# Kernel optimization log

Measured on AMD Instinct MI355X. Metric: run time of the kernel, lower is better.

## Reference

```python
import jax, jax.numpy as jnp
import numpy as np

N = 50000      # nodes
E = 800000     # edges (avg degree 16)
D_IN = 369     # input feature dim
D = 128        # output_dim / GGNN hidden
T = 13         # max_edge_types
STEPS = 8      # GRU propagation steps
G = 256        # graphs in batch


def setup_inputs() -> dict:
    key = jax.random.key(0)
    ks = jax.random.split(key, 13)
    s = 0.05
    return {
        "x": jax.random.normal(ks[0], (N, D_IN), jnp.float32),
        "edge_index": jax.random.randint(ks[1], (2, E), 0, N, dtype=jnp.int64),
        "edge_attr": jax.random.randint(ks[2], (E,), 0, T, dtype=jnp.int64),
        "batch": jnp.sort(jax.random.randint(ks[3], (N,), 0, G, dtype=jnp.int64)),
        "lin_w": jax.random.normal(ks[4], (D_IN, D), jnp.float32) * s,
        "lin_b": jax.random.normal(ks[5], (D,), jnp.float32) * s,
        # per-edge-type GatedGraphConv: weight[t, step] is [D, D]
        "ggnn_w": jax.random.normal(ks[6], (T, STEPS, D, D), jnp.float32) * s,
        # per-edge-type GRUCell params (torch layout: [3*D, D] rows = r,z,n)
        "gru_w_ih": jax.random.normal(ks[7], (T, 3 * D, D), jnp.float32) * s,
        "gru_w_hh": jax.random.normal(ks[8], (T, 3 * D, D), jnp.float32) * s,
        "gru_b_ih": jax.random.normal(ks[9], (T, 3 * D), jnp.float32) * s,
        "gru_b_hh": jax.random.normal(ks[10], (T, 3 * D), jnp.float32) * s,
        "cls_w": jax.random.normal(ks[11], (D, 2), jnp.float32) * s,
        "cls_b": jax.random.normal(ks[12], (2,), jnp.float32) * s,
    }


def reference(x, edge_index, edge_attr, batch,
              lin_w, lin_b, ggnn_w, gru_w_ih, gru_w_hh, gru_b_ih, gru_b_hh,
              cls_w, cls_b):
    n_nodes = x.shape[0]
    h0 = x @ lin_w + lin_b                     # [N, D]; dropout omitted (eval)
    src, dst = edge_index[0], edge_index[1]

    messages = jnp.zeros_like(h0)
    for t in range(T):                          # fixed small set of edge types
        emask = (edge_attr == t).astype(h0.dtype)   # [E] select edges of this type
        w_ih, w_hh = gru_w_ih[t], gru_w_hh[t]
        b_ih, b_hh = gru_b_ih[t], gru_b_hh[t]

        def step(h, w):
            # message passing: aggregate (h @ w)[src] at dst over type-t edges
            xw = h @ w                           # [N, D]
            m = jax.ops.segment_sum(xw[src] * emask[:, None], dst,
                                    num_segments=n_nodes)
            # GRUCell(m, h)
            gi = m @ w_ih.T + b_ih               # [N, 3D]
            gh = h @ w_hh.T + b_hh
            ir, iz, i_n = jnp.split(gi, 3, axis=-1)
            hr, hz, h_n = jnp.split(gh, 3, axis=-1)
            r = jax.nn.sigmoid(ir + hr)
            z = jax.nn.sigmoid(iz + hz)
            n = jnp.tanh(i_n + r * h_n)
            return (1.0 - z) * n + z * h, None

        h_t, _ = jax.lax.scan(step, h0, ggnn_w[t])   # 8 steps
        messages = messages + h_t

    # global_mean_pool over graphs
    sums = jax.ops.segment_sum(messages, batch, num_segments=G)   # [G, D]
    counts = jax.ops.segment_sum(jnp.ones((n_nodes,), messages.dtype), batch,
                                 num_segments=G)
    pooled = sums / jnp.maximum(counts, 1.0)[:, None]
    return pooled @ cls_w + cls_b                                 # [G, 2]
```

## Files before the change

kernel.cpp:

```cpp
#include <hip/hip_runtime.h>
#include <hip/hip_bf16.h>
#include <stdint.h>

typedef __attribute__((ext_vector_type(8))) short   short8;
typedef __attribute__((ext_vector_type(8))) __bf16  bf16x8;
typedef __attribute__((ext_vector_type(4))) float   f32x4;

#define DEV __device__ __forceinline__

DEV float bf2f(uint16_t u){ union{uint32_t i; float f;} v; v.i = ((uint32_t)u)<<16; return v.f; }
DEV uint16_t f2bf(float f){ union{float f; uint32_t i;} v; v.f=f; uint32_t x=v.i;
  return (uint16_t)((x + 0x7fffu + ((x>>16)&1u))>>16); }
DEV float sigmf(float x){ return 1.0f/(1.0f + __expf(-x)); }
DEV float tanhx(float x){ x = fminf(15.f, fmaxf(-15.f, x)); float e = __expf(-2.0f*x);
  return (1.0f-e)/(1.0f+e); }

DEV bf16x8 as_bf(short8 s){ union{ short8 s; bf16x8 b; } u; u.s = s; return u.b; }
DEV f32x4 mfma16(short8 a, short8 b, f32x4 c){
  return __builtin_amdgcn_mfma_f32_16x16x32_bf16(as_bf(a), as_bf(b), c, 0, 0, 0);
}
DEV f32x4 vzero(){ f32x4 v; v[0]=0.f; v[1]=0.f; v[2]=0.f; v[3]=0.f; return v; }

__global__ void cast_bf16_kernel(const float* __restrict__ in, uint16_t* __restrict__ out, int n){
  int i = blockIdx.x*256 + threadIdx.x;
  if (i < n) out[i] = f2bf(in[i]);
}

__global__ void cast_swz_kernel(const float* __restrict__ in, uint16_t* __restrict__ out, int n){
  int i = blockIdx.x*256 + threadIdx.x;
  if (i < n){
    int k = i & 127, row = i >> 7;
    out[(row<<7) + (((k>>3) ^ (row&15))<<3) + (k&7)] = f2bf(in[i]);
  }
}

__global__ void xpad_kernel(const float* __restrict__ x, uint16_t* __restrict__ xb, int rows){
  int i = blockIdx.x*256 + threadIdx.x;
  if (i < rows*384){
    int r = i/384, c = i - r*384;
    xb[i] = (c < 369) ? f2bf(x[r*369 + c]) : (uint16_t)0;
  }
}

__global__ void lwt_kernel(const float* __restrict__ lw, uint16_t* __restrict__ lwT){
  int i = blockIdx.x*256 + threadIdx.x;
  if (i < 128*384){
    int nn = i/384, k = i - nn*384;
    lwT[i] = (k < 369) ? f2bf(lw[k*128 + nn]) : (uint16_t)0;
  }
}

__global__ __launch_bounds__(256,2)
void gemm_bt_kernel(const uint16_t* __restrict__ A, const uint16_t* __restrict__ B,
                    uint16_t* __restrict__ C,
                    int lda, int ldb, int M, int K4,
                    const float* __restrict__ bias, int swz,
                    long sA, long sB, long sC, int divA)
{
  int by = blockIdx.y;
  A += (long)(by/divA)*sA; B += (long)by*sB; C += (long)by*sC;
  int tid = threadIdx.x, lane = tid&63, wave = tid>>6;
  int l15 = lane&15, quad = lane>>4;
  int m0 = blockIdx.x*64 + wave*16;
  f32x4 acc[8];
  #pragma unroll
  for (int nf=0; nf<8; ++nf) acc[nf] = vzero();
  int mrow = min(m0 + l15, M-1);
  const char* arow = (const char*)(A + (long)mrow*lda) + quad*16;
  for (int kk=0; kk<K4; ++kk){
    short8 a = *(const short8*)(arow + kk*64);
    #pragma unroll
    for (int nf=0; nf<8; ++nf){
      const char* brow = (const char*)(B + (long)(nf*16+l15)*ldb) + quad*16;
      short8 b = *(const short8*)(brow + kk*64);
      acc[nf] = mfma16(a, b, acc[nf]);
    }
  }
  #pragma unroll
  for (int nf=0; nf<8; ++nf){
    int col = nf*16 + l15;
    float bb = bias ? bias[col] : 0.0f;
    #pragma unroll
    for (int i=0; i<4; ++i){
      int row = m0 + quad*4 + i;
      if (row < M){
        float v = acc[nf][i] + bb;
        int idx = swz ? (row*128 + (((col>>3)^(row&15))<<3) + (col&7)) : (row*128+col);
        C[idx] = f2bf(v);
      }
    }
  }
}

__global__ void edge_count_kernel(const int* __restrict__ ei, const int* __restrict__ ea,
                                  int* __restrict__ cnt, int E, int n){
  int e = blockIdx.x*256 + threadIdx.x;
  if (e < E){
    int dst = ei[E + e];
    int t = ea[e];
    atomicAdd(&cnt[t*n + dst], 1);
  }
}

__global__ void csr_alloc_kernel(const int* __restrict__ cnt, int* __restrict__ row_start,
                                 int* __restrict__ cursor, int* __restrict__ total, int R){
  __shared__ int wsum[4];
  __shared__ int base;
  int i = blockIdx.x*256 + threadIdx.x;
  int c = (i < R) ? cnt[i] : 0;
  int lane = threadIdx.x & 63, wave = threadIdx.x >> 6;
  int x = c;
  #pragma unroll
  for (int d=1; d<64; d<<=1){ int y = __shfl_up(x, d, 64); if (lane >= d) x += y; }
  if (lane == 63) wsum[wave] = x;
  __syncthreads();
  if (threadIdx.x == 0){
    int s0=wsum[0], s1=wsum[1], s2=wsum[2], s3=wsum[3];
    base = atomicAdd(total, s0+s1+s2+s3);
    wsum[0]=0; wsum[1]=s0; wsum[2]=s0+s1; wsum[3]=s0+s1+s2;
  }
  __syncthreads();
  int st = base + wsum[wave] + (x - c);
  if (i < R){ row_start[i] = st; cursor[i] = st; }
}

__global__ void edge_fill_kernel(const int* __restrict__ ei, const int* __restrict__ ea,
                                 int* __restrict__ cursor, int* __restrict__ csr, int E, int n){
  int e = blockIdx.x*256 + threadIdx.x;
  if (e < E){
    int src = ei[e], dst = ei[E+e], t = ea[e];
    int pos = atomicAdd(&cursor[t*n + dst], 1);
    csr[pos] = src;
  }
}

__global__ __launch_bounds__(256, 2)
void ggnn_step_kernel(const uint16_t* __restrict__ h_in_b,
                      uint16_t* __restrict__ h_out_b,
                      const uint16_t* __restrict__ W1_b,
                      const uint16_t* __restrict__ W2_b,
                      const float* __restrict__ bih_b,
                      const float* __restrict__ bhh_b,
                      const int* __restrict__ row_start_b,
                      const int* __restrict__ row_cnt_b,
                      const int* __restrict__ csr_src,
                      int n, int s, int t_off,
                      long hin_stride, long hout_stride)
{
  __shared__ __align__(16) uint16_t sB[128*128];
  const int t = t_off + blockIdx.y;
  const uint16_t* h_in  = h_in_b  + (long)blockIdx.y*hin_stride;
  uint16_t*       h_out = h_out_b + (long)blockIdx.y*hout_stride;
  const uint16_t* W1s = W1_b + (size_t)(t*8+s)*384*128;
  const uint16_t* W2s = W2_b + (size_t)t*384*128;
  const float* bih = bih_b + t*384;
  const float* bhh = bhh_b + t*384;

  const int tid = threadIdx.x, lane = tid&63, wave = tid>>6;
  const int l15 = lane&15, quad = lane>>4;
  const int rbase = blockIdx.x*64;
  const int ar = rbase + wave*16 + l15;
  const int arc = min(ar, n-1);

  const uint16_t* stp[6] = { W1s, W2s, W1s+2*16384, W2s+2*16384, W1s+16384, W2s+16384 };

  short8 tmp[8];
  {
    const char* g = (const char*)stp[0] + tid*16;
    #pragma unroll
    for (int it=0; it<8; ++it) tmp[it] = *(const short8*)(g + it*4096);
  }

  short8 hfr[4];
  {
    const short8* hrow = (const short8*)(h_in + (long)arc*128);
    #pragma unroll
    for (int kk=0; kk<4; ++kk) hfr[kk] = hrow[kk*4 + quad];
  }

  float acc[32];
  #pragma unroll
  for (int j=0; j<32; ++j) acc[j] = 0.f;
  if (ar < n){
    int st = row_start_b[(size_t)t*n + ar];
    int cn = row_cnt_b  [(size_t)t*n + ar];
    for (int e=0; e<cn; ++e){
      int src = csr_src[st+e];
      const short8* sr = (const short8*)(h_in + (long)src*128);
      #pragma unroll
      for (int kk=0; kk<4; ++kk){
        short8 hv = sr[kk*4+quad];
        #pragma unroll
        for (int j=0; j<8; ++j) acc[kk*8+j] += bf2f((uint16_t)hv[j]);
      }
    }
  }
  short8 afr[4];
  #pragma unroll
  for (int kk=0; kk<4; ++kk){
    #pragma unroll
    for (int j=0; j<8; ++j) afr[kk][j] = (short)f2bf(acc[kk*8+j]);
  }

  auto mma = [&](f32x4* a8, const short8* frag){
    #pragma unroll
    for (int kk=0; kk<4; ++kk){
      int ch = ((kk*4+quad)^l15)<<4;
      short8 a = frag[kk];
      #pragma unroll
      for (int nf=0; nf<8; ++nf){
        short8 b = *(const short8*)((const char*)sB + (nf*16+l15)*256 + ch);
        a8[nf] = mfma16(a, b, a8[nf]);
      }
    }
  };

  f32x4 rg[8], nng[8], zg[8];
  #pragma unroll
  for (int nf=0; nf<8; ++nf){ rg[nf]=vzero(); nng[nf]=vzero(); zg[nf]=vzero(); }

  #pragma unroll
  for (int g=0; g<6; ++g){
    __syncthreads();
    {
      char* l = (char*)sB + tid*16;
      #pragma unroll
      for (int it=0; it<8; ++it) *(short8*)(l + it*4096) = tmp[it];
    }
    __syncthreads();
    if (g < 5){
      const char* gp = (const char*)stp[g+1] + tid*16;
      #pragma unroll
      for (int it=0; it<8; ++it) tmp[it] = *(const short8*)(gp + it*4096);
    }
    if (g == 0)      mma(rg, afr);
    else if (g == 1){
      mma(rg, hfr);
      #pragma unroll
      for (int nf=0; nf<8; ++nf){
        int col = nf*16 + l15;
        float bs = bih[col] + bhh[col];
        #pragma unroll
        for (int i=0; i<4; ++i) rg[nf][i] = sigmf(rg[nf][i] + bs);
      }
    }
    else if (g == 2) mma(nng, afr);
    else if (g == 3){
      f32x4 nh[8];
      #pragma unroll
      for (int nf=0; nf<8; ++nf) nh[nf] = vzero();
      mma(nh, hfr);
      #pragma unroll
      for (int nf=0; nf<8; ++nf){
        int col = nf*16 + l15;
        float bin = bih[256+col], bhn = bhh[256+col];
        #pragma unroll
        for (int i=0; i<4; ++i)
          nng[nf][i] = tanhx(nng[nf][i] + bin + rg[nf][i]*(nh[nf][i] + bhn));
      }
    }
    else if (g == 4) mma(zg, afr);
    else             mma(zg, hfr);
  }

  #pragma unroll
  for (int nf=0; nf<8; ++nf){
    int col = nf*16 + l15;
    float bs = bih[128+col] + bhh[128+col];
    #pragma unroll
    for (int i=0; i<4; ++i){
      int row = rbase + wave*16 + quad*4 + i;
      if (row < n){
        float z = sigmf(zg[nf][i] + bs);
        float hv = bf2f(h_in[(long)row*128 + col]);
        float hnew = nng[nf][i] + z*(hv - nng[nf][i]);
        h_out[(long)row*128 + col] = f2bf(hnew);
      }
    }
  }
}

__global__ void reduce_kernel(const uint16_t* __restrict__ hfin, float* __restrict__ messages,
                              long stride, int nt, int accumulate, int total8){
  int i = blockIdx.x*256 + threadIdx.x;
  if (i < total8){
    float acc[8];
    #pragma unroll
    for (int j=0;j<8;++j) acc[j] = 0.f;
    if (accumulate){
      #pragma unroll
      for (int j=0;j<8;++j) acc[j] = messages[(long)i*8 + j];
    }
    for (int t=0; t<nt; ++t){
      short8 v = *(const short8*)(hfin + (long)t*stride + (long)i*8);
      #pragma unroll
      for (int j=0;j<8;++j) acc[j] += bf2f((uint16_t)v[j]);
    }
    #pragma unroll
    for (int j=0;j<8;++j) messages[(long)i*8 + j] = acc[j];
  }
}

__global__ void pool_kernel(const float* __restrict__ messages, const int* __restrict__ batch,
                            float* __restrict__ sums, int* __restrict__ cntg, int n){
  int id = blockIdx.x*256 + threadIdx.x;
  int col = id & 127;
  int nb = (id >> 7) * 8;
  float acc = 0.f; int curg = -1; int ccount = 0;
  for (int j=0; j<8; ++j){
    int node = nb + j;
    if (node < n){
      int g = batch[node];
      if (g != curg){
        if (curg >= 0){
          atomicAdd(&sums[curg*128+col], acc);
          if (col == 0) atomicAdd(&cntg[curg], ccount);
        }
        curg = g; acc = 0.f; ccount = 0;
      }
      acc += messages[(long)node*128 + col];
      ccount++;
    }
  }
  if (curg >= 0){
    atomicAdd(&sums[curg*128+col], acc);
    if (col == 0) atomicAdd(&cntg[curg], ccount);
  }
}

__global__ void classify_kernel(const float* __restrict__ sums, const int* __restrict__ cntg,
                                const float* __restrict__ cls_w, const float* __restrict__ cls_b,
                                float* __restrict__ out, int G){
  int g = threadIdx.x;
  if (g < G){
    float inv = 1.0f / fmaxf((float)cntg[g], 1.0f);
    float o0 = 0.f, o1 = 0.f;
    for (int d=0; d<128; ++d){
      float p = sums[g*128+d]*inv;
      o0 += p*cls_w[d*2];
      o1 += p*cls_w[d*2+1];
    }
    out[g*2]   = o0 + cls_b[0];
    out[g*2+1] = o1 + cls_b[1];
  }
}

extern "C" void kernel_launch(void* const* d_in, const int* in_sizes, int n_in,
                              void* d_out, int out_size, void* d_ws, size_t ws_size,
                              hipStream_t stream)
{
  const float* x      = (const float*)d_in[0];
  const int*   ei     = (const int*)d_in[1];
  const int*   ea     = (const int*)d_in[2];
  const int*   batch  = (const int*)d_in[3];
  const float* lin_w  = (const float*)d_in[4];
  const float* lin_b  = (const float*)d_in[5];
  const float* ggnn_w = (const float*)d_in[6];
  const float* w_ih   = (const float*)d_in[7];
  const float* w_hh   = (const float*)d_in[8];
  const float* b_ih   = (const float*)d_in[9];
  const float* b_hh   = (const float*)d_in[10];
  const float* cls_w  = (const float*)d_in[11];
  const float* cls_b  = (const float*)d_in[12];
  float* out = (float*)d_out;

  const int N = in_sizes[3];
  const int E = in_sizes[2];
  const int T = in_sizes[9] / 384;
  const int G = out_size / 2;
  const int STEPS = 8;

  struct Layout {
    float *messages, *sums; int *cntg, *total;
    int *cnt, *row_start, *csr;
    uint16_t *W2t, *W1t, *h0;
    uint16_t *hTA, *hTB;
    int *cursor; uint16_t *xb, *lwT, *gwb, *wihb;
    size_t zero_off, zero_len, end;
  };
  auto make_layout = [&](int nh)->Layout{
    Layout L; char* base = (char*)d_ws; char* p = base;
    auto A = [&](size_t b)->char*{ char* r = p; p += (b + 255) & ~(size_t)255; return r; };
    L.messages  = (float*)A((size_t)N*128*4);
    char* z0 = p;
    L.sums      = (float*)A((size_t)G*128*4);
    L.cntg      = (int*)  A((size_t)G*4);
    L.total     = (int*)  A(256);
    L.zero_off = (size_t)(z0 - base); L.zero_len = (size_t)(p - z0);
    L.cnt       = (int*)  A((size_t)T*N*4);
    L.row_start = (int*)  A((size_t)T*N*4);
    L.csr       = (int*)  A((size_t)E*4);
    L.W2t       = (uint16_t*)A((size_t)T*384*128*2);
    L.W1t       = (uint16_t*)A((size_t)T*8*384*128*2);
    L.h0        = (uint16_t*)A((size_t)N*128*2);
    char* R = p;
    size_t hb  = (size_t)N*128*2;
    size_t hba = ((size_t)nh*hb + 255) & ~(size_t)255;
    L.hTA = (uint16_t*)R; L.hTB = (uint16_t*)(R + hba);
    size_t hreg = 2*hba;
    char* q = R;
    auto B = [&](size_t b)->char*{ char* r = q; q += (b + 255) & ~(size_t)255; return r; };
    L.cursor = (int*)     B((size_t)T*N*4);
    L.xb     = (uint16_t*)B((size_t)N*384*2);
    L.lwT    = (uint16_t*)B((size_t)128*384*2);
    L.gwb    = (uint16_t*)B((size_t)T*8*128*128*2);
    L.wihb   = (uint16_t*)B((size_t)T*384*128*2);
    size_t preg = (size_t)(q - R);
    L.end = (size_t)(R - base) + (hreg > preg ? hreg : preg);
    return L;
  };
  int nh = 1;
  { int cand[6] = {13, 8, 6, 4, 3, 2};
    for (int i=0; i<6; ++i){
      int c = cand[i] < T ? cand[i] : T;
      if (make_layout(c).end <= ws_size){ nh = c; break; }
    } }
  Layout L = make_layout(nh);

  hipMemsetAsync((char*)d_ws + L.zero_off, 0, L.zero_len, stream);
  hipMemsetAsync(L.cnt, 0, (size_t)T*N*4, stream);

  const int ngw = T*8*128*128, nwih = T*384*128;
  cast_bf16_kernel<<<(ngw+255)/256, 256, 0, stream>>>(ggnn_w, L.gwb, ngw);
  cast_bf16_kernel<<<(nwih+255)/256, 256, 0, stream>>>(w_ih, L.wihb, nwih);
  cast_swz_kernel <<<(nwih+255)/256, 256, 0, stream>>>(w_hh, L.W2t, nwih);
  xpad_kernel<<<((N*384)+255)/256, 256, 0, stream>>>(x, L.xb, N);
  lwt_kernel<<<(128*384+255)/256, 256, 0, stream>>>(lin_w, L.lwT);

  gemm_bt_kernel<<<dim3(6, T*8), 256, 0, stream>>>(L.wihb, L.gwb, L.W1t, 128, 128, 384, 4,
      nullptr, 1, (long)384*128, (long)128*128, (long)384*128, 8);
  gemm_bt_kernel<<<dim3((N+63)/64, 1), 256, 0, stream>>>(L.xb, L.lwT, L.h0, 384, 384, N, 12,
      lin_b, 0, 0, 0, 0, 1);

  edge_count_kernel<<<(E+255)/256, 256, 0, stream>>>(ei, ea, L.cnt, E, N);
  csr_alloc_kernel <<<(T*N+255)/256, 256, 0, stream>>>(L.cnt, L.row_start, L.cursor, L.total, T*N);
  edge_fill_kernel <<<(E+255)/256, 256, 0, stream>>>(ei, ea, L.cursor, L.csr, E, N);

  const int nblk = (N+63)/64;
  const long hs = (long)N*128;
  const int total8 = N*128/8;
  const int ngroups = (T + nh - 1)/nh;

  for (int gidx=0; gidx<ngroups; ++gidx){
    int t0 = gidx*nh, nt = (T - t0 < nh) ? (T - t0) : nh;
    for (int s=0; s<STEPS; ++s){
      const uint16_t* hin = (s==0) ? L.h0 : ((s&1) ? L.hTB : L.hTA);
      uint16_t* hout = (s&1) ? L.hTA : L.hTB;
      long hin_stride = (s==0) ? 0 : hs;
      ggnn_step_kernel<<<dim3(nblk, nt), 256, 0, stream>>>(
          hin, hout, L.W1t, L.W2t, b_ih, b_hh,
          L.row_start, L.cnt, L.csr, N, s, t0, hin_stride, hs);
    }
    reduce_kernel<<<(total8+255)/256, 256, 0, stream>>>(L.hTA, L.messages, hs, nt,
                                                        (gidx>0) ? 1 : 0, total8);
  }

  pool_kernel<<<((N*128)+2047)/2048, 256, 0, stream>>>(L.messages, batch, L.sums, L.cntg, N);
  classify_kernel<<<1, 256, 0, stream>>>(L.sums, L.cntg, cls_w, cls_b, out, G);
}
```

Before: 3.585 ms.

## Retile GRU step kernel to 2x32-row by 64-col wave tiles

Each wave now computes two 16-row M tiles over a 64-column half instead of one 16-row tile over all 128 columns, so each LDS B fragment load feeds two MFMAs. The cost of this is that every row's edge gather and aggregation is done redundantly by two waves, which doubles neighbour reads. The maximum number of edge types batched per launch also drops from 13 to 7, giving smaller workspace and different launch grouping.

```diff
diff --git a/kernel.cpp b/kernel.cpp
--- a/kernel.cpp
+++ b/kernel.cpp
@@ -159,8 +159,8 @@
   const int tid = threadIdx.x, lane = tid&63, wave = tid>>6;
   const int l15 = lane&15, quad = lane>>4;
   const int rbase = blockIdx.x*64;
-  const int ar = rbase + wave*16 + l15;
-  const int arc = min(ar, n-1);
+  const int r0 = rbase + (wave&1)*32;
+  const int cb = (wave>>1)*64;
 
   const uint16_t* stp[6] = { W1s, W2s, W1s+2*16384, W2s+2*16384, W1s+16384, W2s+16384 };
 
@@ -171,53 +171,61 @@
     for (int it=0; it<8; ++it) tmp[it] = *(const short8*)(g + it*4096);
   }
 
-  short8 hfr[4];
-  {
-    const short8* hrow = (const short8*)(h_in + (long)arc*128);
-    #pragma unroll
-    for (int kk=0; kk<4; ++kk) hfr[kk] = hrow[kk*4 + quad];
-  }
-
-  float acc[32];
-  #pragma unroll
-  for (int j=0; j<32; ++j) acc[j] = 0.f;
-  if (ar < n){
-    int st = row_start_b[(size_t)t*n + ar];
-    int cn = row_cnt_b  [(size_t)t*n + ar];
-    for (int e=0; e<cn; ++e){
-      int src = csr_src[st+e];
-      const short8* sr = (const short8*)(h_in + (long)src*128);
-      #pragma unroll
-      for (int kk=0; kk<4; ++kk){
-        short8 hv = sr[kk*4+quad];
+  short8 hfr[2][4];
+  #pragma unroll
+  for (int mt=0; mt<2; ++mt){
+    const short8* hrow = (const short8*)(h_in + (long)min(r0 + mt*16 + l15, n-1)*128);
+    #pragma unroll
+    for (int kk=0; kk<4; ++kk) hfr[mt][kk] = hrow[kk*4 + quad];
+  }
+
+  short8 afr[2][4];
+  #pragma unroll
+  for (int mt=0; mt<2; ++mt){
+    float acc[32];
+    #pragma unroll
+    for (int j=0; j<32; ++j) acc[j] = 0.f;
+    int ar = r0 + mt*16 + l15;
+    if (ar < n){
+      int st = row_start_b[(size_t)t*n + ar];
+      int cn = row_cnt_b  [(size_t)t*n + ar];
+      for (int e=0; e<cn; ++e){
+        int src = csr_src[st+e];
+        const short8* sr = (const short8*)(h_in + (long)src*128);
         #pragma unroll
-        for (int j=0; j<8; ++j) acc[kk*8+j] += bf2f((uint16_t)hv[j]);
+        for (int kk=0; kk<4; ++kk){
+          short8 hv = sr[kk*4+quad];
+          #pragma unroll
+          for (int j=0; j<8; ++j) acc[kk*8+j] += bf2f((uint16_t)hv[j]);
+        }
       }
     }
-  }
-  short8 afr[4];
-  #pragma unroll
-  for (int kk=0; kk<4; ++kk){
-    #pragma unroll
-    for (int j=0; j<8; ++j) afr[kk][j] = (short)f2bf(acc[kk*8+j]);
-  }
-
-  auto mma = [&](f32x4* a8, const short8* frag){
+    #pragma unroll
+    for (int kk=0; kk<4; ++kk){
+      #pragma unroll
+      for (int j=0; j<8; ++j) afr[mt][kk][j] = (short)f2bf(acc[kk*8+j]);
+    }
+  }
+
+  auto mma = [&](f32x4 (*a8)[4], const short8 (*frag)[4]){
     #pragma unroll
     for (int kk=0; kk<4; ++kk){
       int ch = ((kk*4+quad)^l15)<<4;
-      short8 a = frag[kk];
-      #pragma unroll
-      for (int nf=0; nf<8; ++nf){
-        short8 b = *(const short8*)((const char*)sB + (nf*16+l15)*256 + ch);
-        a8[nf] = mfma16(a, b, a8[nf]);
+      #pragma unroll
+      for (int nf=0; nf<4; ++nf){
+        short8 b = *(const short8*)((const char*)sB + (cb + nf*16 + l15)*256 + ch);
+        #pragma unroll
+        for (int mt=0; mt<2; ++mt)
+          a8[mt][nf] = mfma16(frag[mt][kk], b, a8[mt][nf]);
       }
     }
   };
 
-  f32x4 rg[8], nng[8], zg[8];
-  #pragma unroll
-  for (int nf=0; nf<8; ++nf){ rg[nf]=vzero(); nng[nf]=vzero(); zg[nf]=vzero(); }
+  f32x4 rg[2][4], nng[2][4], zg[2][4];
+  #pragma unroll
+  for (int mt=0; mt<2; ++mt)
+    #pragma unroll
+    for (int nf=0; nf<4; ++nf){ rg[mt][nf]=vzero(); nng[mt][nf]=vzero(); zg[mt][nf]=vzero(); }
 
   #pragma unroll
   for (int g=0; g<6; ++g){
@@ -237,47 +245,55 @@
     else if (g == 1){
       mma(rg, hfr);
       #pragma unroll
-      for (int nf=0; nf<8; ++nf){
-        int col = nf*16 + l15;
-        float bs = bih[col] + bhh[col];
+      for (int mt=0; mt<2; ++mt)
         #pragma unroll
-        for (int i=0; i<4; ++i) rg[nf][i] = sigmf(rg[nf][i] + bs);
-      }
+        for (int nf=0; nf<4; ++nf){
+          int col = cb + nf*16 + l15;
+          float bs = bih[col] + bhh[col];
+          #pragma unroll
+          for (int i=0; i<4; ++i) rg[mt][nf][i] = sigmf(rg[mt][nf][i] + bs);
+        }
     }
     else if (g == 2) mma(nng, afr);
     else if (g == 3){
-      f32x4 nh[8];
-      #pragma unroll
-      for (int nf=0; nf<8; ++nf) nh[nf] = vzero();
+      f32x4 nh[2][4];
+      #pragma unroll
+      for (int mt=0; mt<2; ++mt)
+        #pragma unroll
+        for (int nf=0; nf<4; ++nf) nh[mt][nf] = vzero();
       mma(nh, hfr);
       #pragma unroll
-      for (int nf=0; nf<8; ++nf){
-        int col = nf*16 + l15;
-        float bin = bih[256+col], bhn = bhh[256+col];
+      for (int mt=0; mt<2; ++mt)
         #pragma unroll
-        for (int i=0; i<4; ++i)
-          nng[nf][i] = tanhx(nng[nf][i] + bin + rg[nf][i]*(nh[nf][i] + bhn));
-      }
+        for (int nf=0; nf<4; ++nf){
+          int col = cb + nf*16 + l15;
+          float bin = bih[256+col], bhn = bhh[256+col];
+          #pragma unroll
+          for (int i=0; i<4; ++i)
+            nng[mt][nf][i] = tanhx(nng[mt][nf][i] + bin + rg[mt][nf][i]*(nh[mt][nf][i] + bhn));
+        }
     }
     else if (g == 4) mma(zg, afr);
     else             mma(zg, hfr);
   }
 
   #pragma unroll
-  for (int nf=0; nf<8; ++nf){
-    int col = nf*16 + l15;
-    float bs = bih[128+col] + bhh[128+col];
-    #pragma unroll
-    for (int i=0; i<4; ++i){
-      int row = rbase + wave*16 + quad*4 + i;
-      if (row < n){
-        float z = sigmf(zg[nf][i] + bs);
-        float hv = bf2f(h_in[(long)row*128 + col]);
-        float hnew = nng[nf][i] + z*(hv - nng[nf][i]);
-        h_out[(long)row*128 + col] = f2bf(hnew);
+  for (int mt=0; mt<2; ++mt)
+    #pragma unroll
+    for (int nf=0; nf<4; ++nf){
+      int col = cb + nf*16 + l15;
+      float bs = bih[128+col] + bhh[128+col];
+      #pragma unroll
+      for (int i=0; i<4; ++i){
+        int row = r0 + mt*16 + quad*4 + i;
+        if (row < n){
+          float z = sigmf(zg[mt][nf][i] + bs);
+          float hv = bf2f(h_in[(long)row*128 + col]);
+          float hnew = nng[mt][nf][i] + z*(hv - nng[mt][nf][i]);
+          h_out[(long)row*128 + col] = f2bf(hnew);
+        }
       }
     }
-  }
 }
 
 __global__ void reduce_kernel(const uint16_t* __restrict__ hfin, float* __restrict__ messages,
@@ -410,7 +426,7 @@
     return L;
   };
   int nh = 1;
-  { int cand[6] = {13, 8, 6, 4, 3, 2};
+  { int cand[6] = {7, 6, 5, 4, 3, 2};
     for (int i=0; i<6; ++i){
       int c = cand[i] < T ? cand[i] : T;
       if (make_layout(c).end <= ws_size){ nh = c; break; }
```

New measurement: 4.651 ms. +29.7%, slower.

## Split neighbor aggregation into separate gather kernel before GRU step

Applied to the files above, without the earlier changes.

Moves the CSR neighbor-sum out of the fused GGNN step kernel into a dedicated agg_kernel that assigns 16 threads per row, so the gather runs with high parallelism and without the register pressure of the MFMA kernel. The step kernel then reads the precomputed bf16 aggregate instead of gathering. This adds an extra write and read of an N×128 buffer per type per step, plus a third h buffer that shrinks the max edge types processed concurrently (candidates capped at 5).

```diff
diff --git a/kernel.cpp b/kernel.cpp
--- a/kernel.cpp
+++ b/kernel.cpp
@@ -134,23 +134,51 @@
   }
 }
 
+__global__ void agg_kernel(const uint16_t* __restrict__ h_in_b,
+                           uint16_t* __restrict__ agg_b,
+                           const int* __restrict__ row_start_b,
+                           const int* __restrict__ row_cnt_b,
+                           const int* __restrict__ csr_src,
+                           int n, int t_off, long hin_stride)
+{
+  const int t = t_off + blockIdx.y;
+  const uint16_t* h_in = h_in_b + (long)blockIdx.y*hin_stride;
+  uint16_t* agg = agg_b + (long)blockIdx.y*((long)n*128);
+  int id = blockIdx.x*256 + threadIdx.x;
+  int row = id >> 4, c = (id & 15) * 8;
+  if (row < n){
+    int st = row_start_b[(size_t)t*n + row];
+    int cn = row_cnt_b  [(size_t)t*n + row];
+    float acc[8] = {0,0,0,0,0,0,0,0};
+    for (int e=0; e<cn; ++e){
+      int src = csr_src[st + e];
+      short8 v = *(const short8*)(h_in + (long)src*128 + c);
+      #pragma unroll
+      for (int j=0; j<8; ++j) acc[j] += bf2f((uint16_t)v[j]);
+    }
+    short8 pk;
+    #pragma unroll
+    for (int j=0; j<8; ++j) pk[j] = (short)f2bf(acc[j]);
+    *(short8*)(agg + (long)row*128 + c) = pk;
+  }
+}
+
 __global__ __launch_bounds__(256, 2)
 void ggnn_step_kernel(const uint16_t* __restrict__ h_in_b,
+                      const uint16_t* __restrict__ agg_b,
                       uint16_t* __restrict__ h_out_b,
                       const uint16_t* __restrict__ W1_b,
                       const uint16_t* __restrict__ W2_b,
                       const float* __restrict__ bih_b,
                       const float* __restrict__ bhh_b,
-                      const int* __restrict__ row_start_b,
-                      const int* __restrict__ row_cnt_b,
-                      const int* __restrict__ csr_src,
                       int n, int s, int t_off,
-                      long hin_stride, long hout_stride)
+                      long hin_stride, long hstride)
 {
   __shared__ __align__(16) uint16_t sB[128*128];
   const int t = t_off + blockIdx.y;
-  const uint16_t* h_in  = h_in_b  + (long)blockIdx.y*hin_stride;
-  uint16_t*       h_out = h_out_b + (long)blockIdx.y*hout_stride;
+  const uint16_t* h_in = h_in_b + (long)blockIdx.y*hin_stride;
+  const uint16_t* agg  = agg_b  + (long)blockIdx.y*hstride;
+  uint16_t*       h_out= h_out_b+ (long)blockIdx.y*hstride;
   const uint16_t* W1s = W1_b + (size_t)(t*8+s)*384*128;
   const uint16_t* W2s = W2_b + (size_t)t*384*128;
   const float* bih = bih_b + t*384;
@@ -171,35 +199,12 @@
     for (int it=0; it<8; ++it) tmp[it] = *(const short8*)(g + it*4096);
   }
 
-  short8 hfr[4];
+  short8 hfr[4], afr[4];
   {
     const short8* hrow = (const short8*)(h_in + (long)arc*128);
-    #pragma unroll
-    for (int kk=0; kk<4; ++kk) hfr[kk] = hrow[kk*4 + quad];
-  }
-
-  float acc[32];
-  #pragma unroll
-  for (int j=0; j<32; ++j) acc[j] = 0.f;
-  if (ar < n){
-    int st = row_start_b[(size_t)t*n + ar];
-    int cn = row_cnt_b  [(size_t)t*n + ar];
-    for (int e=0; e<cn; ++e){
-      int src = csr_src[st+e];
-      const short8* sr = (const short8*)(h_in + (long)src*128);
-      #pragma unroll
-      for (int kk=0; kk<4; ++kk){
-        short8 hv = sr[kk*4+quad];
-        #pragma unroll
-        for (int j=0; j<8; ++j) acc[kk*8+j] += bf2f((uint16_t)hv[j]);
-      }
-    }
-  }
-  short8 afr[4];
-  #pragma unroll
-  for (int kk=0; kk<4; ++kk){
-    #pragma unroll
-    for (int j=0; j<8; ++j) afr[kk][j] = (short)f2bf(acc[kk*8+j]);
+    const short8* arow = (const short8*)(agg  + (long)arc*128);
+    #pragma unroll
+    for (int kk=0; kk<4; ++kk){ hfr[kk] = hrow[kk*4 + quad]; afr[kk] = arow[kk*4 + quad]; }
   }
 
   auto mma = [&](f32x4* a8, const short8* frag){
@@ -374,7 +379,7 @@
     float *messages, *sums; int *cntg, *total;
     int *cnt, *row_start, *csr;
     uint16_t *W2t, *W1t, *h0;
-    uint16_t *hTA, *hTB;
+    uint16_t *hTA, *hTB, *agg;
     int *cursor; uint16_t *xb, *lwT, *gwb, *wihb;
     size_t zero_off, zero_len, end;
   };
@@ -396,8 +401,8 @@
     char* R = p;
     size_t hb  = (size_t)N*128*2;
     size_t hba = ((size_t)nh*hb + 255) & ~(size_t)255;
-    L.hTA = (uint16_t*)R; L.hTB = (uint16_t*)(R + hba);
-    size_t hreg = 2*hba;
+    L.hTA = (uint16_t*)R; L.hTB = (uint16_t*)(R + hba); L.agg = (uint16_t*)(R + 2*hba);
+    size_t hreg = 3*hba;
     char* q = R;
     auto B = [&](size_t b)->char*{ char* r = q; q += (b + 255) & ~(size_t)255; return r; };
     L.cursor = (int*)     B((size_t)T*N*4);
@@ -410,8 +415,8 @@
     return L;
   };
   int nh = 1;
-  { int cand[6] = {13, 8, 6, 4, 3, 2};
-    for (int i=0; i<6; ++i){
+  { int cand[4] = {5, 4, 3, 2};
+    for (int i=0; i<4; ++i){
       int c = cand[i] < T ? cand[i] : T;
       if (make_layout(c).end <= ws_size){ nh = c; break; }
     } }
@@ -437,6 +442,7 @@
   edge_fill_kernel <<<(E+255)/256, 256, 0, stream>>>(ei, ea, L.cursor, L.csr, E, N);
 
   const int nblk = (N+63)/64;
+  const int ablk = (N*16 + 255)/256;
   const long hs = (long)N*128;
   const int total8 = N*128/8;
   const int ngroups = (T + nh - 1)/nh;
@@ -447,9 +453,11 @@
       const uint16_t* hin = (s==0) ? L.h0 : ((s&1) ? L.hTB : L.hTA);
       uint16_t* hout = (s&1) ? L.hTA : L.hTB;
       long hin_stride = (s==0) ? 0 : hs;
+      agg_kernel<<<dim3(ablk, nt), 256, 0, stream>>>(
+          hin, L.agg, L.row_start, L.cnt, L.csr, N, t0, hin_stride);
       ggnn_step_kernel<<<dim3(nblk, nt), 256, 0, stream>>>(
-          hin, hout, L.W1t, L.W2t, b_ih, b_hh,
-          L.row_start, L.cnt, L.csr, N, s, t0, hin_stride, hs);
+          hin, L.agg, hout, L.W1t, L.W2t, b_ih, b_hh,
+          N, s, t0, hin_stride, hs);
     }
     reduce_kernel<<<(total8+255)/256, 256, 0, stream>>>(L.hTA, L.messages, hs, nt,
                                                         (gidx>0) ? 1 : 0, total8);
```

Result: no change. 3.642 ms (+1.6%).
